# Optimization experiments

Measured on AMD Instinct MI355X. Metric: run time of the kernel, lower is better.

The kernel has to match this reference:

```python
import jax, jax.numpy as jnp
import numpy as np

NUM_CLASSES = 10
OUT_DIM = 16
NUM_ROUTING = 3
ROUTING_BIAS = 0.1


def _squash(s):
    # s: [B, C, D]; norm over last (out_capsule) dim, matches torch norm(dim=2)
    norm = jnp.linalg.norm(s, axis=2, keepdims=True)
    # s / (1+norm^2) / norm * norm^2 == s * norm / (1 + norm^2)
    return s * norm / (1.0 + norm * norm)


def setup_inputs() -> dict:
    key = jax.random.key(0)
    k1, k2 = jax.random.split(key)
    B, N, IN_DIM = 256, 2304, 8
    x = jax.random.normal(k1, (B, N, IN_DIM), dtype=jnp.float32)
    # kaiming-normal-ish init for W [N, in_dim, classes*out_dim]
    W = jax.random.normal(k2, (N, IN_DIM, NUM_CLASSES * OUT_DIM), dtype=jnp.float32) * np.sqrt(2.0 / IN_DIM)
    return {"x": x, "W": W}


def reference(x, W):
    B, N, _ = x.shape
    # broadcast-multiply+sum in original == per-capsule matmul
    u_hat = jnp.einsum('bni,nio->bno', x, W).reshape(B, N, NUM_CLASSES, OUT_DIM)
    u_hat_sg = jax.lax.stop_gradient(u_hat)
    b = jnp.zeros((B, N, NUM_CLASSES), dtype=x.dtype)
    v = None
    for i in range(NUM_ROUTING):
        c = jax.nn.softmax(b, axis=2)  # [B, N, C]
        if i == NUM_ROUTING - 1:
            s = jnp.einsum('bnc,bncd->bcd', c, u_hat) + ROUTING_BIAS
            v = _squash(s)
        else:
            s = jnp.einsum('bnc,bncd->bcd', c, u_hat_sg) + ROUTING_BIAS
            # NOTE: original updates b with pre-squash s (not v) -- kept faithful
            b = b + jnp.einsum('bncd,bcd->bnc', u_hat_sg, s)
    return v
```

## Files before the change

### kernel.cpp

```cpp
#include <hip/hip_runtime.h>
#include <math.h>

#define B_TOT   256
#define N_TOT   2304
#define IN_DIM  8
#define NC      10
#define OD      16
#define CD      160
#define RBIAS   0.1f

#define BTILE    64
#define NS       128
#define NPB      (N_TOT / NS)
#define NTHREADS 640
#define XR       (NPB * IN_DIM + 4)
#define LB       72
#define WROW     (IN_DIM * CD)
#define SRAW     (B_TOT * CD)

#define NXCD     8

template <int FIRST>
__global__ __launch_bounds__(NTHREADS) void routing_round(
    const float* __restrict__ x,
    const float* __restrict__ W,
    const float* __restrict__ S_acc,
    float* __restrict__ rawT)
{
    __shared__ float sh_x[BTILE * XR];
    __shared__ float sh_lg[2][NC * LB];

    const int tid = threadIdx.x;

    const int o      = blockIdx.x;
    const int xcd    = o & (NXCD - 1);
    const int r      = o >> 3;
    const int cuslot = r & 31;
    const int pairid = r >> 5;
    const int ySlab  = xcd * 16 + (cuslot & 15);
    const int b0     = ((cuslot >> 4) * 2 + pairid) * BTILE;
    const int n0     = ySlab * NPB;

    const int b   = tid & 63;
    const int cu  = __builtin_amdgcn_readfirstlane(tid >> 6);

    {
        const int XT4 = BTILE * (NPB * IN_DIM / 4);
        for (int k = tid; k < XT4; k += NTHREADS) {
            int bb   = k / (NPB * 2);
            int off4 = k - bb * (NPB * 2);
            float4 v = *(const float4*)(x + ((size_t)(b0 + bb) * N_TOT + n0) * IN_DIM + off4 * 4);
            *(float4*)(&sh_x[bb * XR + off4 * 4]) = v;
        }
    }

    float S[OD];
    if (!FIRST) {
        const float4* sp = (const float4*)(S_acc + (size_t)(b0 + b) * CD + cu * OD);
        #pragma unroll
        for (int q = 0; q < 4; q++) ((float4*)S)[q] = sp[q];
    }

    float acc[OD];
    #pragma unroll
    for (int d = 0; d < OD; d++) acc[d] = 0.f;

    __syncthreads();

    const float* Wc = W + cu * OD;

    for (int nn = 0; nn < NPB; nn++) {
        float xf[IN_DIM];
        {
            const float4* xp = (const float4*)(&sh_x[b * XR + nn * IN_DIM]);
            ((float4*)xf)[0] = xp[0];
            ((float4*)xf)[1] = xp[1];
        }

        const float* Wn = Wc + (size_t)(n0 + nn) * WROW;
        float u[OD];
        #pragma unroll
        for (int d = 0; d < OD; d++) u[d] = xf[0] * Wn[d];
        #pragma unroll
        for (int i = 1; i < IN_DIM; i++) {
            const float* Wi = Wn + i * CD;
            #pragma unroll
            for (int d = 0; d < OD; d++) u[d] = fmaf(xf[i], Wi[d], u[d]);
        }

        if (!FIRST) {
            const int cur = nn & 1;
            float lg = 0.f;
            #pragma unroll
            for (int d = 0; d < OD; d++) lg = fmaf(u[d], S[d], lg);
            sh_lg[cur][cu * LB + b] = lg;
            __syncthreads();

            float m = -1e30f;
            float row[NC];
            #pragma unroll
            for (int k = 0; k < NC; k++) {
                row[k] = sh_lg[cur][k * LB + b];
                m = fmaxf(m, row[k]);
            }
            float den = 0.f;
            #pragma unroll
            for (int k = 0; k < NC; k++) den += __expf(row[k] - m);
            float cw = __expf(lg - m) / den;

            #pragma unroll
            for (int d = 0; d < OD; d++) acc[d] = fmaf(cw, u[d], acc[d]);
        } else {
            #pragma unroll
            for (int d = 0; d < OD; d++) acc[d] += u[d];
        }
    }

    float* dst = rawT + b0 + b;
    #pragma unroll
    for (int d = 0; d < OD; d++)
        atomicAdd(dst + (size_t)(cu * OD + d) * B_TOT, acc[d]);
}

__global__ __launch_bounds__(256) void zero_raws(float4* __restrict__ p)
{
    p[(size_t)blockIdx.x * 256 + threadIdx.x] = (float4){0.f, 0.f, 0.f, 0.f};
}

__global__ __launch_bounds__(256) void finalize_round(
    const float* __restrict__ rawT,
    float* __restrict__ S_acc,
    float* __restrict__ v_out,
    int mode)
{
    const int p   = blockIdx.x * 256 + threadIdx.x;
    const int b   = p / 40;
    const int rem = p - b * 40;
    const int cd0 = rem * 4;

    float t0 = rawT[(size_t)(cd0 + 0) * B_TOT + b];
    float t1 = rawT[(size_t)(cd0 + 1) * B_TOT + b];
    float t2 = rawT[(size_t)(cd0 + 2) * B_TOT + b];
    float t3 = rawT[(size_t)(cd0 + 3) * B_TOT + b];

    if (mode == 0) {
        float4 o = { t0 * 0.1f + RBIAS, t1 * 0.1f + RBIAS,
                     t2 * 0.1f + RBIAS, t3 * 0.1f + RBIAS };
        ((float4*)S_acc)[p] = o;
    } else if (mode == 1) {
        float4 o = ((const float4*)S_acc)[p];
        o.x += t0 + RBIAS; o.y += t1 + RBIAS;
        o.z += t2 + RBIAS; o.w += t3 + RBIAS;
        ((float4*)S_acc)[p] = o;
    } else {
        const float s0 = t0 + RBIAS, s1 = t1 + RBIAS;
        const float s2 = t2 + RBIAS, s3 = t3 + RBIAS;
        float ss = s0 * s0 + s1 * s1 + s2 * s2 + s3 * s3;
        ss += __shfl_xor(ss, 1, 64);
        ss += __shfl_xor(ss, 2, 64);
        const float norm = sqrtf(ss);
        const float k2 = norm / (1.0f + ss);
        float4 v = { s0 * k2, s1 * k2, s2 * k2, s3 * k2 };
        ((float4*)v_out)[p] = v;
    }
}

extern "C" void kernel_launch(void* const* d_in, const int* in_sizes, int n_in,
                              void* d_out, int out_size, void* d_ws, size_t ws_size,
                              hipStream_t stream) {
    const float* x = (const float*)d_in[0];
    const float* W = (const float*)d_in[1];
    float* out = (float*)d_out;

    float* raw0  = (float*)d_ws;
    float* raw1  = raw0 + SRAW;
    float* raw2  = raw1 + SRAW;
    float* S_acc = raw2 + SRAW;

    const dim3 rgrid(512);

    zero_raws<<<120, 256, 0, stream>>>((float4*)raw0);

    routing_round<1><<<rgrid, NTHREADS, 0, stream>>>(x, W, S_acc, raw0);
    finalize_round<<<40, 256, 0, stream>>>(raw0, S_acc, out, 0);

    routing_round<0><<<rgrid, NTHREADS, 0, stream>>>(x, W, S_acc, raw1);
    finalize_round<<<40, 256, 0, stream>>>(raw1, S_acc, out, 1);

    routing_round<0><<<rgrid, NTHREADS, 0, stream>>>(x, W, S_acc, raw2);
    finalize_round<<<40, 256, 0, stream>>>(raw2, S_acc, out, 2);
}
```

Baseline: 202.1 us.

## Compute u_hat with split-bf16 MFMA and double-buffered shared W tiles

Replaces the scalar FMA computation of u_hat with 16x16x32 bf16 MFMA instructions. Both x and W are split into hi/lo bf16 pairs so the products keep near-fp32 accuracy. Each block now covers all 256 batch rows for a slice of 9 capsules, staging W into a double-buffered shared tile so it is converted once and reused across the batch. The softmax reduction moves from a shared-memory round trip to wave shuffles. In exchange the kernel pays for the splitting arithmetic, uses 1024-thread blocks with a large shared x buffer, and keeps a barrier on every capsule iteration.

```diff
diff --git a/kernel.cpp b/kernel.cpp
--- a/kernel.cpp
+++ b/kernel.cpp
@@ -9,117 +9,179 @@
 #define CD      160
 #define RBIAS   0.1f
 
-#define BTILE    64
-#define NS       128
-#define NPB      (N_TOT / NS)
-#define NTHREADS 640
-#define XR       (NPB * IN_DIM + 4)
-#define LB       72
-#define WROW     (IN_DIM * CD)
-#define SRAW     (B_TOT * CD)
-
-#define NXCD     8
+#define NSL     256
+#define NPB     (N_TOT / NSL)
+#define NTH     1024
+#define XRS     76
+#define WPR     196
+#define WROW    (IN_DIM * CD)
+#define SRAW    (B_TOT * CD)
+#define NXCD    8
+
+typedef __attribute__((ext_vector_type(8))) short bf16x8;
+typedef __attribute__((ext_vector_type(4))) float f32x4;
+
+__device__ __forceinline__ unsigned int rne_hi(unsigned int b) {
+    return (b + 0x7FFFu + ((b >> 16) & 1u)) & 0xFFFF0000u;
+}
+__device__ __forceinline__ void split2(float f, unsigned int& h, unsigned int& l) {
+    unsigned int xb = __float_as_uint(f);
+    h = rne_hi(xb);
+    float fl = f - __uint_as_float(h);
+    l = __float_as_uint(fl) & 0xFFFF0000u;
+}
 
 template <int FIRST>
-__global__ __launch_bounds__(NTHREADS) void routing_round(
+__global__ __launch_bounds__(NTH, 4) void routing_round(
     const float* __restrict__ x,
     const float* __restrict__ W,
     const float* __restrict__ S_acc,
     float* __restrict__ rawT)
 {
-    __shared__ float sh_x[BTILE * XR];
-    __shared__ float sh_lg[2][NC * LB];
-
-    const int tid = threadIdx.x;
-
-    const int o      = blockIdx.x;
-    const int xcd    = o & (NXCD - 1);
-    const int r      = o >> 3;
-    const int cuslot = r & 31;
-    const int pairid = r >> 5;
-    const int ySlab  = xcd * 16 + (cuslot & 15);
-    const int b0     = ((cuslot >> 4) * 2 + pairid) * BTILE;
-    const int n0     = ySlab * NPB;
-
-    const int b   = tid & 63;
-    const int cu  = __builtin_amdgcn_readfirstlane(tid >> 6);
-
+    __shared__ __align__(16) float        sh_x[B_TOT * XRS];
+    __shared__ __align__(16) unsigned int sh_wp[2][8 * WPR];
+
+    const int tid  = threadIdx.x;
+    const int lane = tid & 63;
+    const int w    = tid >> 6;
+    const int l    = lane & 15;
+    const int g    = lane >> 4;
+
+    const int bid   = blockIdx.x;
+    const int xcd   = bid & (NXCD - 1);
+    const int ySlab = xcd * 32 + (bid >> 3);
+    const int n0    = ySlab * NPB;
+
+    const int bglob = w * 16 + l;
+
+    for (int k = tid; k < B_TOT * 18; k += NTH) {
+        int bb = k / 18, off4 = k - bb * 18;
+        float4 v = *(const float4*)(x + ((size_t)bb * N_TOT + n0) * IN_DIM + off4 * 4);
+        *(float4*)(&sh_x[bb * XRS + off4 * 4]) = v;
+    }
     {
-        const int XT4 = BTILE * (NPB * IN_DIM / 4);
-        for (int k = tid; k < XT4; k += NTHREADS) {
-            int bb   = k / (NPB * 2);
-            int off4 = k - bb * (NPB * 2);
-            float4 v = *(const float4*)(x + ((size_t)(b0 + bb) * N_TOT + n0) * IN_DIM + off4 * 4);
-            *(float4*)(&sh_x[bb * XR + off4 * 4]) = v;
-        }
-    }
-
-    float S[OD];
+        const float* Wr = W + (size_t)n0 * WROW;
+        for (int e = tid; e < WROW; e += NTH) {
+            int i = e / 160, r = e - i * 160;
+            int c = r >> 4, d = r & 15;
+            unsigned int h, lo; split2(Wr[e], h, lo);
+            sh_wp[0][i * WPR + d * 12 + c] = (h >> 16) | lo;
+        }
+    }
+
+    float S[NC][4];
     if (!FIRST) {
-        const float4* sp = (const float4*)(S_acc + (size_t)(b0 + b) * CD + cu * OD);
         #pragma unroll
-        for (int q = 0; q < 4; q++) ((float4*)S)[q] = sp[q];
-    }
-
-    float acc[OD];
+        for (int c = 0; c < NC; c++)
+            #pragma unroll
+            for (int rg = 0; rg < 4; rg++)
+                S[c][rg] = S_acc[(size_t)bglob * CD + c * OD + 4 * g + rg];
+    }
+
+    f32x4 acc[NC];
     #pragma unroll
-    for (int d = 0; d < OD; d++) acc[d] = 0.f;
+    for (int c = 0; c < NC; c++) acc[c] = (f32x4){0.f, 0.f, 0.f, 0.f};
 
     __syncthreads();
 
-    const float* Wc = W + cu * OD;
-
     for (int nn = 0; nn < NPB; nn++) {
-        float xf[IN_DIM];
+        const int cur = nn & 1;
+
+        if (nn + 1 < NPB) {
+            const float* Wr = W + (size_t)(n0 + nn + 1) * WROW;
+            for (int e = tid; e < WROW; e += NTH) {
+                int i = e / 160, r = e - i * 160;
+                int c = r >> 4, d = r & 15;
+                unsigned int h, lo; split2(Wr[e], h, lo);
+                sh_wp[cur ^ 1][i * WPR + d * 12 + c] = (h >> 16) | lo;
+            }
+        }
+
+        union { unsigned int d[4]; bf16x8 v; } Bx;
         {
-            const float4* xp = (const float4*)(&sh_x[b * XR + nn * IN_DIM]);
-            ((float4*)xf)[0] = xp[0];
-            ((float4*)xf)[1] = xp[1];
-        }
-
-        const float* Wn = Wc + (size_t)(n0 + nn) * WROW;
-        float u[OD];
+            float x0 = sh_x[bglob * XRS + nn * IN_DIM + g];
+            float x1 = sh_x[bglob * XRS + nn * IN_DIM + g + 4];
+            unsigned int h0, l0, h1, l1;
+            split2(x0, h0, l0); split2(x1, h1, l1);
+            Bx.d[0] = (h0 >> 16) | h0;
+            Bx.d[1] = (l0 >> 16) | l0;
+            Bx.d[2] = (h1 >> 16) | h1;
+            Bx.d[3] = (l1 >> 16) | l1;
+        }
+
+        const unsigned int* wp0 = &sh_wp[cur][g       * WPR + l * 12];
+        const unsigned int* wp1 = &sh_wp[cur][(g + 4) * WPR + l * 12];
+        uint4 a0 = *(const uint4*)(wp0);
+        uint4 a1 = *(const uint4*)(wp0 + 4);
+        uint2 a2 = *(const uint2*)(wp0 + 8);
+        uint4 b0 = *(const uint4*)(wp1);
+        uint4 b1 = *(const uint4*)(wp1 + 4);
+        uint2 b2 = *(const uint2*)(wp1 + 8);
+
+#define MK_A(pa, pb) Af.d[0] = (pa); Af.d[1] = (pa); Af.d[2] = (pb); Af.d[3] = (pb)
+
+        if (!FIRST) {
+            union { unsigned int d[4]; bf16x8 v; } Af;
+            float lg[NC];
+#define LG1(idx, pa, pb) { MK_A(pa, pb);                                     \
+            f32x4 u = __builtin_amdgcn_mfma_f32_16x16x32_bf16(               \
+                          Af.v, Bx.v, (f32x4){0.f,0.f,0.f,0.f}, 0, 0, 0);    \
+            lg[idx] = u[0]*S[idx][0] + u[1]*S[idx][1]                        \
+                    + u[2]*S[idx][2] + u[3]*S[idx][3]; }
+            LG1(0, a0.x, b0.x) LG1(1, a0.y, b0.y) LG1(2, a0.z, b0.z)
+            LG1(3, a0.w, b0.w) LG1(4, a1.x, b1.x) LG1(5, a1.y, b1.y)
+            LG1(6, a1.z, b1.z) LG1(7, a1.w, b1.w) LG1(8, a2.x, b2.x)
+            LG1(9, a2.y, b2.y)
+#undef LG1
+            #pragma unroll
+            for (int c = 0; c < NC; c++) {
+                float t = lg[c];
+                t += __shfl_xor(t, 16, 64);
+                t += __shfl_xor(t, 32, 64);
+                lg[c] = t;
+            }
+            float m = lg[0];
+            #pragma unroll
+            for (int c = 1; c < NC; c++) m = fmaxf(m, lg[c]);
+            float den = 0.f;
+            #pragma unroll
+            for (int c = 0; c < NC; c++) { lg[c] = __expf(lg[c] - m); den += lg[c]; }
+            const float rden = 1.f / den;
+#define AC2(idx, pa, pb) { MK_A(pa, pb);                                     \
+            f32x4 u = __builtin_amdgcn_mfma_f32_16x16x32_bf16(               \
+                          Af.v, Bx.v, (f32x4){0.f,0.f,0.f,0.f}, 0, 0, 0);    \
+            float cwv = lg[idx] * rden;                                      \
+            acc[idx][0] = fmaf(cwv, u[0], acc[idx][0]);                      \
+            acc[idx][1] = fmaf(cwv, u[1], acc[idx][1]);                      \
+            acc[idx][2] = fmaf(cwv, u[2], acc[idx][2]);                      \
+            acc[idx][3] = fmaf(cwv, u[3], acc[idx][3]); }
+            AC2(0, a0.x, b0.x) AC2(1, a0.y, b0.y) AC2(2, a0.z, b0.z)
+            AC2(3, a0.w, b0.w) AC2(4, a1.x, b1.x) AC2(5, a1.y, b1.y)
+            AC2(6, a1.z, b1.z) AC2(7, a1.w, b1.w) AC2(8, a2.x, b2.x)
+            AC2(9, a2.y, b2.y)
+#undef AC2
+        } else {
+            union { unsigned int d[4]; bf16x8 v; } Af;
+#define AC0(idx, pa, pb) { MK_A(pa, pb);                                     \
+            acc[idx] = __builtin_amdgcn_mfma_f32_16x16x32_bf16(              \
+                           Af.v, Bx.v, acc[idx], 0, 0, 0); }
+            AC0(0, a0.x, b0.x) AC0(1, a0.y, b0.y) AC0(2, a0.z, b0.z)
+            AC0(3, a0.w, b0.w) AC0(4, a1.x, b1.x) AC0(5, a1.y, b1.y)
+            AC0(6, a1.z, b1.z) AC0(7, a1.w, b1.w) AC0(8, a2.x, b2.x)
+            AC0(9, a2.y, b2.y)
+#undef AC0
+        }
+#undef MK_A
+
+        __syncthreads();
+    }
+
+    #pragma unroll
+    for (int c = 0; c < NC; c++)
         #pragma unroll
-        for (int d = 0; d < OD; d++) u[d] = xf[0] * Wn[d];
-        #pragma unroll
-        for (int i = 1; i < IN_DIM; i++) {
-            const float* Wi = Wn + i * CD;
-            #pragma unroll
-            for (int d = 0; d < OD; d++) u[d] = fmaf(xf[i], Wi[d], u[d]);
-        }
-
-        if (!FIRST) {
-            const int cur = nn & 1;
-            float lg = 0.f;
-            #pragma unroll
-            for (int d = 0; d < OD; d++) lg = fmaf(u[d], S[d], lg);
-            sh_lg[cur][cu * LB + b] = lg;
-            __syncthreads();
-
-            float m = -1e30f;
-            float row[NC];
-            #pragma unroll
-            for (int k = 0; k < NC; k++) {
-                row[k] = sh_lg[cur][k * LB + b];
-                m = fmaxf(m, row[k]);
-            }
-            float den = 0.f;
-            #pragma unroll
-            for (int k = 0; k < NC; k++) den += __expf(row[k] - m);
-            float cw = __expf(lg - m) / den;
-
-            #pragma unroll
-            for (int d = 0; d < OD; d++) acc[d] = fmaf(cw, u[d], acc[d]);
-        } else {
-            #pragma unroll
-            for (int d = 0; d < OD; d++) acc[d] += u[d];
-        }
-    }
-
-    float* dst = rawT + b0 + b;
-    #pragma unroll
-    for (int d = 0; d < OD; d++)
-        atomicAdd(dst + (size_t)(cu * OD + d) * B_TOT, acc[d]);
+        for (int rg = 0; rg < 4; rg++)
+            atomicAdd(rawT + (size_t)(c * OD + 4 * g + rg) * B_TOT + bglob,
+                      acc[c][rg]);
 }
 
 __global__ __launch_bounds__(256) void zero_raws(float4* __restrict__ p)
@@ -177,16 +239,16 @@
     float* raw2  = raw1 + SRAW;
     float* S_acc = raw2 + SRAW;
 
-    const dim3 rgrid(512);
+    const dim3 rgrid(NSL);
 
     zero_raws<<<120, 256, 0, stream>>>((float4*)raw0);
 
-    routing_round<1><<<rgrid, NTHREADS, 0, stream>>>(x, W, S_acc, raw0);
+    routing_round<1><<<rgrid, NTH, 0, stream>>>(x, W, S_acc, raw0);
     finalize_round<<<40, 256, 0, stream>>>(raw0, S_acc, out, 0);
 
-    routing_round<0><<<rgrid, NTHREADS, 0, stream>>>(x, W, S_acc, raw1);
+    routing_round<0><<<rgrid, NTH, 0, stream>>>(x, W, S_acc, raw1);
     finalize_round<<<40, 256, 0, stream>>>(raw1, S_acc, out, 1);
 
-    routing_round<0><<<rgrid, NTHREADS, 0, stream>>>(x, W, S_acc, raw2);
+    routing_round<0><<<rgrid, NTH, 0, stream>>>(x, W, S_acc, raw2);
     finalize_round<<<40, 256, 0, stream>>>(raw2, S_acc, out, 2);
 }
```

Measured after the change: 287.1 us. 42.1% more time.
